# Optimization experiments

Hardware: AMD Instinct MI355X
Metric: run time of the kernel (lower is better)

Reference implementation:

```python
import jax, jax.numpy as jnp
import numpy as np

N_NODES = 100000
N_RAND_EDGES = 1600000
EPS = 1e-12


def setup_inputs() -> dict:
    key = jax.random.key(0)
    k_x, k_w1, k_w2, k_r, k_c = jax.random.split(key, 5)
    X = jax.random.normal(k_x, (N_NODES, 256), dtype=jnp.float32)
    # Linear weights stored as [in, out] so forward is X @ W (bias=False)
    W1 = jax.random.normal(k_w1, (256, 128), dtype=jnp.float32) * 0.05
    W2 = jax.random.normal(k_w2, (128, 64), dtype=jnp.float32) * 0.05
    row = jax.random.randint(k_r, (N_RAND_EDGES,), 0, N_NODES, dtype=jnp.int32)
    col = jax.random.randint(k_c, (N_RAND_EDGES,), 0, N_NODES, dtype=jnp.int32)
    loops = jnp.arange(N_NODES, dtype=jnp.int32)  # self-loops (A has self-loops)
    edge_row = jnp.concatenate([row, loops])
    edge_col = jnp.concatenate([col, loops])
    return {"X": X, "W1": W1, "W2": W2, "edge_row": edge_row, "edge_col": edge_col}


def _norm_edge_weights(edge_row, edge_col):
    # degrees = row-sums of A (all values are 1.0)
    deg = jax.ops.segment_sum(jnp.ones_like(edge_row, dtype=jnp.float32), edge_row,
                              num_segments=N_NODES)
    d_inv_sqrt = 1.0 / jnp.clip(jnp.sqrt(deg), EPS)
    # A_hat = D^-1/2 A D^-1/2  <=>  per-edge weight
    return d_inv_sqrt[edge_row] * d_inv_sqrt[edge_col]


def _spmm(w, edge_row, edge_col, X):
    # (A_hat @ X)[i] = sum_{e: row_e = i} w_e * X[col_e]
    return jax.ops.segment_sum(w[:, None] * X[edge_col], edge_row,
                               num_segments=N_NODES)


def reference(X, W1, W2, edge_row, edge_col):
    w = _norm_edge_weights(edge_row, edge_col)
    # layer 0: GraphConvolution -> ReLU (dropout is identity in eval mode)
    H = jax.nn.relu(_spmm(w, edge_row, edge_col, X @ W1))
    # layer 1: GraphConvolution (logits)
    out = _spmm(w, edge_row, edge_col, H @ W2)
    return out
```

## Files before the change

### kernel.cpp

```cpp
#include <hip/hip_runtime.h>
#include <hip/hip_bf16.h>


typedef __attribute__((ext_vector_type(8))) short short8;
typedef __attribute__((ext_vector_type(4))) float floatx4;
typedef __attribute__((ext_vector_type(2))) float floatx2;

static __device__ __forceinline__ ushort f32_to_bf16_bits(float f) {
    union { ushort u; __hip_bfloat16 b; } cv;
    cv.b = __float2bfloat16(f);
    return cv.u;
}
static __device__ __forceinline__ float bf16lo_to_f32(uint u) {
    return __uint_as_float(u << 16);
}
static __device__ __forceinline__ float bf16hi_to_f32(uint u) {
    return __uint_as_float(u & 0xffff0000u);
}
static __device__ __forceinline__ uint pack2bf(float a, float b) {
    return (uint)f32_to_bf16_bits(a) | ((uint)f32_to_bf16_bits(b) << 16);
}

#define CSR_EPB 8192
#define SPMM_CHUNK 2048

__global__ __launch_bounds__(256) void scan_phase1_kernel(
    const int* __restrict__ in, int* __restrict__ out,
    int* __restrict__ block_total, int n) {
    __shared__ int tsum[256];
    int t = threadIdx.x;
    int base = blockIdx.x * 1024 + t * 4;
    int v0 = (base + 0 < n) ? in[base + 0] : 0;
    int v1 = (base + 1 < n) ? in[base + 1] : 0;
    int v2 = (base + 2 < n) ? in[base + 2] : 0;
    int v3 = (base + 3 < n) ? in[base + 3] : 0;
    tsum[t] = v0 + v1 + v2 + v3;
    __syncthreads();
    for (int off = 1; off < 256; off <<= 1) {
        int x = (t >= off) ? tsum[t - off] : 0;
        __syncthreads();
        tsum[t] += x;
        __syncthreads();
    }
    if (t == 255) block_total[blockIdx.x] = tsum[255];
    int run = (t == 0) ? 0 : tsum[t - 1];
    if (base + 0 < n) out[base + 0] = run; run += v0;
    if (base + 1 < n) out[base + 1] = run; run += v1;
    if (base + 2 < n) out[base + 2] = run; run += v2;
    if (base + 3 < n) out[base + 3] = run;
}

__global__ __launch_bounds__(256) void scan_phase2_kernel(
    const int* __restrict__ block_total, int* __restrict__ block_offset, int G) {
    __shared__ int s[256];
    int t = threadIdx.x;
    s[t] = (t < G) ? block_total[t] : 0;
    __syncthreads();
    for (int off = 1; off < 256; off <<= 1) {
        int x = (t >= off) ? s[t - off] : 0;
        __syncthreads();
        s[t] += x;
        __syncthreads();
    }
    if (t < G) block_offset[t] = (t == 0) ? 0 : s[t - 1];
    if (t == 0) block_offset[G] = s[255];
}

__global__ __launch_bounds__(256) void scan_phase3_kernel(
    int* __restrict__ arr, const int* __restrict__ block_offset, int n, int G) {
    int i = blockIdx.x * blockDim.x + threadIdx.x;
    if (i < n) arr[i] += block_offset[i >> 10];
    if (i == 0) arr[n] = block_offset[G];
}


__global__ __launch_bounds__(256) void edge_hist_kernel(
    const int* __restrict__ keys, int* __restrict__ histG, int E, int nblk) {
    __shared__ int h[256];
    int t = threadIdx.x;
    h[t] = 0;
    __syncthreads();
    int base = blockIdx.x * CSR_EPB;
    int end = min(base + CSR_EPB, E);
    for (int i = base + t; i < end; i += 256)
        atomicAdd(&h[keys[i] >> 9], 1);
    __syncthreads();
    histG[t * nblk + blockIdx.x] = h[t];
}

__global__ __launch_bounds__(256) void edge_bin_kernel(
    const int* __restrict__ rows, const int* __restrict__ colsIn,
    const int* __restrict__ offG, int* __restrict__ binP, int E, int nblk) {
    __shared__ int cur[256];
    int t = threadIdx.x;
    cur[t] = offG[t * nblk + blockIdx.x];
    __syncthreads();
    int base = blockIdx.x * CSR_EPB;
    int end = min(base + CSR_EPB, E);
    for (int i = base + t; i < end; i += 256) {
        int r = rows[i], c = colsIn[i];
        int p = atomicAdd(&cur[r >> 9], 1);
        binP[p] = ((r & 511) << 17) | c;
    }
}

__global__ __launch_bounds__(256) void deg_dinv_from_bin_kernel(
    const int* __restrict__ binP, const int* __restrict__ offG,
    int* __restrict__ deg, float* __restrict__ dinv, int E, int nblk, int N) {
    __shared__ int cnt[512];
    int b = blockIdx.x;
    int rbase = b << 9;
    if (rbase >= N) return;
    int t = threadIdx.x;
    for (int i = t; i < 512; i += 256) cnt[i] = 0;
    __syncthreads();
    int bs = offG[b * nblk];
    int be = (b + 1 < 256) ? offG[(b + 1) * nblk] : E;
    for (int e = bs + t; e < be; e += 256)
        atomicAdd(&cnt[binP[e] >> 17], 1);
    __syncthreads();
    for (int i = t; i < 512; i += 256) {
        int r = rbase + i;
        if (r < N) {
            int d = cnt[i];
            deg[r] = d;
            dinv[r] = 1.0f / sqrtf(fmaxf((float)d, 1e-24f));
        }
    }
}

__global__ __launch_bounds__(256) void edge_scatter_kernel(
    const int* __restrict__ binP, const int* __restrict__ offG,
    const int* __restrict__ row_ptr, int* __restrict__ csr_col,
    int E, int nblk, int N) {
    __shared__ int cur[512];
    int b = blockIdx.x;
    int rbase = b << 9;
    if (rbase >= N) return;
    int t = threadIdx.x;
    for (int i = t; i < 512; i += 256) {
        int r = rbase + i;
        cur[i] = (r < N) ? row_ptr[r] : 0;
    }
    __syncthreads();
    int bs = offG[b * nblk];
    int be = (b + 1 < 256) ? offG[(b + 1) * nblk] : E;
    for (int e = bs + t; e < be; e += 256) {
        int pk = binP[e];
        int rl = pk >> 17;
        int c = pk & 0x1ffff;
        int p = atomicAdd(&cur[rl], 1);
        csr_col[p] = c;
    }
}

__global__ void cast_weights_kernel(const float* __restrict__ W1, const float* __restrict__ W2,
                                    ushort* __restrict__ W1t, ushort* __restrict__ W2t) {
    int i = blockIdx.x * blockDim.x + threadIdx.x;
    if (i < 256 * 128) {
        int n = i >> 8, k = i & 255;
        W1t[i] = f32_to_bf16_bits(W1[k * 128 + n]);
    } else {
        int j = i - 256 * 128;
        if (j < 128 * 64) {
            int n = j >> 7, k = j & 127;
            W2t[j] = f32_to_bf16_bits(W2[k * 64 + n]);
        }
    }
}

template <int KTOT, int NCOLS, bool AF32>
__global__ __launch_bounds__(256) void gemm_mfma_kernel(
    const void* __restrict__ Aptr, const ushort* __restrict__ Bt,
    const float* __restrict__ dinv, ushort* __restrict__ Cbf, int M) {
    constexpr int KP = 128;
    constexpr int COLT = NCOLS / 16;
    __shared__ ushort Bs[NCOLS][KP + 8];
    int tid = threadIdx.x;
    int wave = tid >> 6, lane = tid & 63;
    int quad = lane >> 4, l16 = lane & 15;
    int row0 = blockIdx.x * 64;
    int rowA = row0 + wave * 16 + l16;
    int rowAc = min(rowA, M - 1);

    floatx4 acc[COLT];
#pragma unroll
    for (int t = 0; t < COLT; t++) acc[t] = (floatx4){0.f, 0.f, 0.f, 0.f};

    for (int kp = 0; kp < KTOT; kp += KP) {
        for (int u = tid; u < NCOLS * (KP / 8); u += 256) {
            int n = u / (KP / 8);
            int k8 = (u % (KP / 8)) * 8;
            *(short8*)&Bs[n][k8] = *(const short8*)(Bt + (size_t)n * KTOT + kp + k8);
        }
        __syncthreads();
#pragma unroll
        for (int kc = 0; kc < KP / 32; kc++) {
            int kk = kp + kc * 32 + quad * 8;
            short8 a;
            if (AF32) {
                const float* ap = (const float*)Aptr + (size_t)rowAc * KTOT + kk;
#pragma unroll
                for (int j = 0; j < 8; j++) a[j] = (short)f32_to_bf16_bits(ap[j]);
            } else {
                a = *(const short8*)((const ushort*)Aptr + (size_t)rowAc * KTOT + kk);
            }
#pragma unroll
            for (int t = 0; t < COLT; t++) {
                short8 b = *(const short8*)&Bs[t * 16 + l16][kc * 32 + quad * 8];
                acc[t] = __builtin_amdgcn_mfma_f32_16x16x32_bf16(a, b, acc[t], 0, 0, 0);
            }
        }
        __syncthreads();
    }

#pragma unroll
    for (int r = 0; r < 4; r++) {
        int row = row0 + wave * 16 + quad * 4 + r;
        if (row < M) {
            float dv = dinv[row];
#pragma unroll
            for (int t = 0; t < COLT; t++)
                Cbf[(size_t)row * NCOLS + t * 16 + l16] = f32_to_bf16_bits(dv * acc[t][r]);
        }
    }
}

__global__ __launch_bounds__(256) void spmm_f128_kernel(
    const int* __restrict__ row_ptr, const int* __restrict__ cols,
    const float* __restrict__ dinv, const ushort* __restrict__ Xin,
    ushort* __restrict__ Yout, int n) {
    __shared__ int cstage[SPMM_CHUNK];
    int r0 = blockIdx.x * 16;
    int tid = threadIdx.x;
    int wv = tid >> 6;
    int lane = tid & 63;
    int g = lane >> 4, lg = lane & 15;
    int row = r0 + wv * 4 + g;
    bool ok = row < n;
    int rc = ok ? row : (n - 1);
    int beg = row_ptr[rc];
    int end = ok ? row_ptr[rc + 1] : beg;
    int bbeg = row_ptr[r0];
    int bend = row_ptr[min(r0 + 16, n)];

    floatx2 acc2[4];
#pragma unroll
    for (int i = 0; i < 4; i++) acc2[i] = (floatx2){0.f, 0.f};

    const ushort* xb = Xin + lg * 8;

#define ACC_DW(U, D)                                            \
    {                                                            \
        floatx2 v_;                                              \
        v_.x = bf16lo_to_f32(U);                                 \
        v_.y = bf16hi_to_f32(U);                                 \
        acc2[D] += v_;                                           \
    }
#define ACC_U4(UU)                                               \
    ACC_DW(UU.x, 0) ACC_DW(UU.y, 1) ACC_DW(UU.z, 2) ACC_DW(UU.w, 3)

    for (int cb = bbeg; cb < bend; cb += SPMM_CHUNK) {
        int ce = min(cb + SPMM_CHUNK, bend);
        __syncthreads();
        for (int i = cb + tid; i < ce; i += 256)
            cstage[i - cb] = cols[i];
        __syncthreads();
        int s = max(beg, cb), t_ = min(end, ce);
        int e = s;
        for (; e + 4 <= t_; e += 4) {
            int c0 = cstage[e - cb], c1 = cstage[e + 1 - cb];
            int c2 = cstage[e + 2 - cb], c3 = cstage[e + 3 - cb];
            uint4 u0 = *(const uint4*)(xb + (size_t)c0 * 128);
            uint4 u1 = *(const uint4*)(xb + (size_t)c1 * 128);
            uint4 u2 = *(const uint4*)(xb + (size_t)c2 * 128);
            uint4 u3 = *(const uint4*)(xb + (size_t)c3 * 128);
            ACC_U4(u0) ACC_U4(u1) ACC_U4(u2) ACC_U4(u3)
        }
        for (; e < t_; e++) {
            int c = cstage[e - cb];
            uint4 u = *(const uint4*)(xb + (size_t)c * 128);
            ACC_U4(u)
        }
    }
#undef ACC_U4
#undef ACC_DW

    if (ok) {
        float dv = dinv[row];
        float a0 = fmaxf(dv * acc2[0].x, 0.f), a1 = fmaxf(dv * acc2[0].y, 0.f);
        float a2 = fmaxf(dv * acc2[1].x, 0.f), a3 = fmaxf(dv * acc2[1].y, 0.f);
        float a4 = fmaxf(dv * acc2[2].x, 0.f), a5 = fmaxf(dv * acc2[2].y, 0.f);
        float a6 = fmaxf(dv * acc2[3].x, 0.f), a7 = fmaxf(dv * acc2[3].y, 0.f);
        uint4 o;
        o.x = pack2bf(a0, a1);
        o.y = pack2bf(a2, a3);
        o.z = pack2bf(a4, a5);
        o.w = pack2bf(a6, a7);
        *(uint4*)(Yout + (size_t)row * 128 + lg * 8) = o;
    }
}

__global__ __launch_bounds__(256) void spmm_f64_kernel(
    const int* __restrict__ row_ptr, const int* __restrict__ cols,
    const float* __restrict__ dinv, const ushort* __restrict__ Xin,
    float* __restrict__ Yout, int n) {
    __shared__ int cstage[SPMM_CHUNK];
    int r0 = blockIdx.x * 16;
    int tid = threadIdx.x;
    int wv = tid >> 6;
    int lane = tid & 63;
    int g = lane >> 4, lg = lane & 15;
    int row = r0 + wv * 4 + g;
    bool ok = row < n;
    int rc = ok ? row : (n - 1);
    int beg = row_ptr[rc];
    int end = ok ? row_ptr[rc + 1] : beg;
    int bbeg = row_ptr[r0];
    int bend = row_ptr[min(r0 + 16, n)];

    floatx2 acc2[2];
    acc2[0] = (floatx2){0.f, 0.f};
    acc2[1] = (floatx2){0.f, 0.f};

    const ushort* xb = Xin + lg * 4;

#define ACC_DW(U, D)                                            \
    {                                                            \
        floatx2 v_;                                              \
        v_.x = bf16lo_to_f32(U);                                 \
        v_.y = bf16hi_to_f32(U);                                 \
        acc2[D] += v_;                                           \
    }
#define ACC_U2(UU) ACC_DW(UU.x, 0) ACC_DW(UU.y, 1)

    for (int cb = bbeg; cb < bend; cb += SPMM_CHUNK) {
        int ce = min(cb + SPMM_CHUNK, bend);
        __syncthreads();
        for (int i = cb + tid; i < ce; i += 256)
            cstage[i - cb] = cols[i];
        __syncthreads();
        int s = max(beg, cb), t_ = min(end, ce);
        int e = s;
        for (; e + 4 <= t_; e += 4) {
            int c0 = cstage[e - cb], c1 = cstage[e + 1 - cb];
            int c2 = cstage[e + 2 - cb], c3 = cstage[e + 3 - cb];
            uint2 u0 = *(const uint2*)(xb + (size_t)c0 * 64);
            uint2 u1 = *(const uint2*)(xb + (size_t)c1 * 64);
            uint2 u2 = *(const uint2*)(xb + (size_t)c2 * 64);
            uint2 u3 = *(const uint2*)(xb + (size_t)c3 * 64);
            ACC_U2(u0) ACC_U2(u1) ACC_U2(u2) ACC_U2(u3)
        }
        for (; e < t_; e++) {
            int c = cstage[e - cb];
            uint2 u = *(const uint2*)(xb + (size_t)c * 64);
            ACC_U2(u)
        }
    }
#undef ACC_U2
#undef ACC_DW

    if (ok) {
        float dv = dinv[row];
        float4 o = make_float4(dv * acc2[0].x, dv * acc2[0].y,
                               dv * acc2[1].x, dv * acc2[1].y);
        *(float4*)(Yout + (size_t)row * 64 + lg * 4) = o;
    }
}


extern "C" void kernel_launch(void* const* d_in, const int* in_sizes, int n_in,
                              void* d_out, int out_size, void* d_ws, size_t ws_size,
                              hipStream_t stream) {
    const float* X  = (const float*)d_in[0];
    const float* W1 = (const float*)d_in[1];
    const float* W2 = (const float*)d_in[2];
    const int* erow = (const int*)d_in[3];
    const int* ecol = (const int*)d_in[4];

    const int N = in_sizes[0] / 256;
    const int E = in_sizes[3];
    const int G = (N + 1023) >> 10;

    const int nblk = (E + CSR_EPB - 1) / CSR_EPB;
    const int SL = 256 * nblk;
    const int GS = (SL + 1023) >> 10;
    const int GMAX = (G > GS) ? G : GS;

    char* ws = (char*)d_ws;
    size_t off = 0;
    auto carve = [&](size_t bytes) -> char* {
        char* p = ws + off;
        off += (bytes + 255) & ~(size_t)255;
        return p;
    };
    int*    deg       = (int*)   carve((size_t)N * 4);
    float*  dinv      = (float*) carve((size_t)N * 4);
    int*    row_ptr   = (int*)   carve((size_t)(N + 1) * 4);
    int*    blk_total = (int*)   carve((size_t)GMAX * 4);
    int*    blk_off   = (int*)   carve((size_t)(GMAX + 1) * 4);
    int*    offG      = (int*)   carve((size_t)(SL + 1) * 4);
    size_t binP_bytes = (size_t)E * 4;
    size_t xw1_bytes  = (size_t)N * 128 * 2;
    char*  uni        = carve(binP_bytes > xw1_bytes ? binP_bytes : xw1_bytes);
    int*    binP      = (int*)uni;
    ushort* XW1       = (ushort*)uni;
    int*    csr_col   = (int*)   carve((size_t)E * 4);
    ushort* W1t       = (ushort*)carve((size_t)256 * 128 * 2);
    ushort* W2t       = (ushort*)carve((size_t)128 * 64 * 2);
    ushort* H         = (ushort*)carve((size_t)N * 128 * 2);
    ushort* HW2       = (ushort*)carve((size_t)N * 64 * 2);

    edge_hist_kernel<<<nblk, 256, 0, stream>>>(erow, offG, E, nblk);
    scan_phase1_kernel<<<GS, 256, 0, stream>>>(offG, offG, blk_total, SL);
    scan_phase2_kernel<<<1, 256, 0, stream>>>(blk_total, blk_off, GS);
    scan_phase3_kernel<<<(SL + 255) / 256, 256, 0, stream>>>(offG, blk_off, SL, GS);
    edge_bin_kernel<<<nblk, 256, 0, stream>>>(erow, ecol, offG, binP, E, nblk);

    deg_dinv_from_bin_kernel<<<256, 256, 0, stream>>>(binP, offG, deg, dinv, E, nblk, N);
    scan_phase1_kernel<<<G, 256, 0, stream>>>(deg, row_ptr, blk_total, N);
    scan_phase2_kernel<<<1, 256, 0, stream>>>(blk_total, blk_off, G);
    scan_phase3_kernel<<<(N + 255) / 256, 256, 0, stream>>>(row_ptr, blk_off, N, G);

    edge_scatter_kernel<<<256, 256, 0, stream>>>(binP, offG, row_ptr, csr_col, E, nblk, N);

    cast_weights_kernel<<<(256 * 128 + 128 * 64 + 255) / 256, 256, 0, stream>>>(W1, W2, W1t, W2t);

    gemm_mfma_kernel<256, 128, true><<<(N + 63) / 64, 256, 0, stream>>>(
        (const void*)X, W1t, dinv, XW1, N);

    spmm_f128_kernel<<<(N + 15) / 16, 256, 0, stream>>>(row_ptr, csr_col, dinv, XW1, H, N);

    gemm_mfma_kernel<128, 64, false><<<(N + 63) / 64, 256, 0, stream>>>(
        (const void*)H, W2t, dinv, HW2, N);

    spmm_f64_kernel<<<(N + 15) / 16, 256, 0, stream>>>(row_ptr, csr_col, dinv, HW2, (float*)d_out, N);
}
```

Measured before the change: 356.2 us.

## Fuse layer-1 SpMM with second GEMM, merge cast into histogram, drop scan pass

The first SpMM now keeps its ReLU output tile in shared memory and immediately multiplies it by W2 with MFMA, writing HW2 directly. This removes the H buffer round trip and one GEMM launch. The weight cast is folded into the histogram kernel as extra blocks, and the offG scan's phase-3 pass is dropped by adding the block offset at each consumer. The SpMM inner loops gain an 8-way unroll and the staging chunk is halved. The costs are more shared memory and extra W2 staging in every SpMM block, plus lower per-block parallelism for the fused GEMM.

New measurement: 348.2 us. 1.02x faster.

```diff
diff --git a/kernel.cpp b/kernel.cpp
--- a/kernel.cpp
+++ b/kernel.cpp
@@ -22,7 +22,7 @@
 }
 
 #define CSR_EPB 8192
-#define SPMM_CHUNK 2048
+#define SPMM_CHUNK 1024
 
 __global__ __launch_bounds__(256) void scan_phase1_kernel(
     const int* __restrict__ in, int* __restrict__ out,
@@ -73,27 +73,45 @@
     if (i == 0) arr[n] = block_offset[G];
 }
 
-
-__global__ __launch_bounds__(256) void edge_hist_kernel(
-    const int* __restrict__ keys, int* __restrict__ histG, int E, int nblk) {
+__global__ __launch_bounds__(256) void edge_hist_cast_kernel(
+    const int* __restrict__ keys, int* __restrict__ histG, int E, int nblk,
+    const float* __restrict__ W1, const float* __restrict__ W2,
+    ushort* __restrict__ W1t, ushort* __restrict__ W2t) {
+    int b = blockIdx.x;
+    if (b >= nblk) {
+        int i = (b - nblk) * 256 + threadIdx.x;
+        if (i < 256 * 128) {
+            int n = i >> 8, k = i & 255;
+            W1t[i] = f32_to_bf16_bits(W1[k * 128 + n]);
+        } else {
+            int j = i - 256 * 128;
+            if (j < 128 * 64) {
+                int n = j >> 7, k = j & 127;
+                W2t[j] = f32_to_bf16_bits(W2[k * 64 + n]);
+            }
+        }
+        return;
+    }
     __shared__ int h[256];
     int t = threadIdx.x;
     h[t] = 0;
     __syncthreads();
-    int base = blockIdx.x * CSR_EPB;
+    int base = b * CSR_EPB;
     int end = min(base + CSR_EPB, E);
     for (int i = base + t; i < end; i += 256)
         atomicAdd(&h[keys[i] >> 9], 1);
     __syncthreads();
-    histG[t * nblk + blockIdx.x] = h[t];
+    histG[t * nblk + b] = h[t];
 }
 
 __global__ __launch_bounds__(256) void edge_bin_kernel(
     const int* __restrict__ rows, const int* __restrict__ colsIn,
-    const int* __restrict__ offG, int* __restrict__ binP, int E, int nblk) {
+    const int* __restrict__ offG, const int* __restrict__ blk_off1,
+    int* __restrict__ binP, int E, int nblk) {
     __shared__ int cur[256];
     int t = threadIdx.x;
-    cur[t] = offG[t * nblk + blockIdx.x];
+    int idx = t * nblk + blockIdx.x;
+    cur[t] = offG[idx] + blk_off1[idx >> 10];
     __syncthreads();
     int base = blockIdx.x * CSR_EPB;
     int end = min(base + CSR_EPB, E);
@@ -106,6 +124,7 @@
 
 __global__ __launch_bounds__(256) void deg_dinv_from_bin_kernel(
     const int* __restrict__ binP, const int* __restrict__ offG,
+    const int* __restrict__ blk_off1,
     int* __restrict__ deg, float* __restrict__ dinv, int E, int nblk, int N) {
     __shared__ int cnt[512];
     int b = blockIdx.x;
@@ -114,8 +133,13 @@
     int t = threadIdx.x;
     for (int i = t; i < 512; i += 256) cnt[i] = 0;
     __syncthreads();
-    int bs = offG[b * nblk];
-    int be = (b + 1 < 256) ? offG[(b + 1) * nblk] : E;
+    int i0 = b * nblk;
+    int bs = offG[i0] + blk_off1[i0 >> 10];
+    int be = E;
+    if (b + 1 < 256) {
+        int i1 = (b + 1) * nblk;
+        be = offG[i1] + blk_off1[i1 >> 10];
+    }
     for (int e = bs + t; e < be; e += 256)
         atomicAdd(&cnt[binP[e] >> 17], 1);
     __syncthreads();
@@ -131,6 +155,7 @@
 
 __global__ __launch_bounds__(256) void edge_scatter_kernel(
     const int* __restrict__ binP, const int* __restrict__ offG,
+    const int* __restrict__ blk_off1,
     const int* __restrict__ row_ptr, int* __restrict__ csr_col,
     int E, int nblk, int N) {
     __shared__ int cur[512];
@@ -143,29 +168,19 @@
         cur[i] = (r < N) ? row_ptr[r] : 0;
     }
     __syncthreads();
-    int bs = offG[b * nblk];
-    int be = (b + 1 < 256) ? offG[(b + 1) * nblk] : E;
+    int i0 = b * nblk;
+    int bs = offG[i0] + blk_off1[i0 >> 10];
+    int be = E;
+    if (b + 1 < 256) {
+        int i1 = (b + 1) * nblk;
+        be = offG[i1] + blk_off1[i1 >> 10];
+    }
     for (int e = bs + t; e < be; e += 256) {
         int pk = binP[e];
         int rl = pk >> 17;
         int c = pk & 0x1ffff;
         int p = atomicAdd(&cur[rl], 1);
         csr_col[p] = c;
-    }
-}
-
-__global__ void cast_weights_kernel(const float* __restrict__ W1, const float* __restrict__ W2,
-                                    ushort* __restrict__ W1t, ushort* __restrict__ W2t) {
-    int i = blockIdx.x * blockDim.x + threadIdx.x;
-    if (i < 256 * 128) {
-        int n = i >> 8, k = i & 255;
-        W1t[i] = f32_to_bf16_bits(W1[k * 128 + n]);
-    } else {
-        int j = i - 256 * 128;
-        if (j < 128 * 64) {
-            int n = j >> 7, k = j & 127;
-            W2t[j] = f32_to_bf16_bits(W2[k * 64 + n]);
-        }
     }
 }
 
@@ -226,16 +241,19 @@
     }
 }
 
-__global__ __launch_bounds__(256) void spmm_f128_kernel(
+__global__ __launch_bounds__(256) void spmm_gemm2_kernel(
     const int* __restrict__ row_ptr, const int* __restrict__ cols,
-    const float* __restrict__ dinv, const ushort* __restrict__ Xin,
-    ushort* __restrict__ Yout, int n) {
+    const float* __restrict__ dinv, const ushort* __restrict__ XW1,
+    const ushort* __restrict__ W2t, ushort* __restrict__ HW2, int n) {
     __shared__ int cstage[SPMM_CHUNK];
-    int r0 = blockIdx.x * 16;
+    __shared__ ushort W2s[64][136];
+    __shared__ ushort Hs[16][136];
+
     int tid = threadIdx.x;
     int wv = tid >> 6;
     int lane = tid & 63;
     int g = lane >> 4, lg = lane & 15;
+    int r0 = blockIdx.x * 16;
     int row = r0 + wv * 4 + g;
     bool ok = row < n;
     int rc = ok ? row : (n - 1);
@@ -244,11 +262,16 @@
     int bbeg = row_ptr[r0];
     int bend = row_ptr[min(r0 + 16, n)];
 
+    for (int u = tid; u < 64 * 16; u += 256) {
+        int nn = u >> 4, k8 = (u & 15) * 8;
+        *(short8*)&W2s[nn][k8] = *(const short8*)(W2t + nn * 128 + k8);
+    }
+
     floatx2 acc2[4];
 #pragma unroll
     for (int i = 0; i < 4; i++) acc2[i] = (floatx2){0.f, 0.f};
 
-    const ushort* xb = Xin + lg * 8;
+    const ushort* xb = XW1 + lg * 8;
 
 #define ACC_DW(U, D)                                            \
     {                                                            \
@@ -268,6 +291,22 @@
         __syncthreads();
         int s = max(beg, cb), t_ = min(end, ce);
         int e = s;
+        for (; e + 8 <= t_; e += 8) {
+            int c0 = cstage[e - cb], c1 = cstage[e + 1 - cb];
+            int c2 = cstage[e + 2 - cb], c3 = cstage[e + 3 - cb];
+            int c4 = cstage[e + 4 - cb], c5 = cstage[e + 5 - cb];
+            int c6 = cstage[e + 6 - cb], c7 = cstage[e + 7 - cb];
+            uint4 u0 = *(const uint4*)(xb + (size_t)c0 * 128);
+            uint4 u1 = *(const uint4*)(xb + (size_t)c1 * 128);
+            uint4 u2 = *(const uint4*)(xb + (size_t)c2 * 128);
+            uint4 u3 = *(const uint4*)(xb + (size_t)c3 * 128);
+            uint4 u4 = *(const uint4*)(xb + (size_t)c4 * 128);
+            uint4 u5 = *(const uint4*)(xb + (size_t)c5 * 128);
+            uint4 u6 = *(const uint4*)(xb + (size_t)c6 * 128);
+            uint4 u7 = *(const uint4*)(xb + (size_t)c7 * 128);
+            ACC_U4(u0) ACC_U4(u1) ACC_U4(u2) ACC_U4(u3)
+            ACC_U4(u4) ACC_U4(u5) ACC_U4(u6) ACC_U4(u7)
+        }
         for (; e + 4 <= t_; e += 4) {
             int c0 = cstage[e - cb], c1 = cstage[e + 1 - cb];
             int c2 = cstage[e + 2 - cb], c3 = cstage[e + 3 - cb];
@@ -286,8 +325,8 @@
 #undef ACC_U4
 #undef ACC_DW
 
-    if (ok) {
-        float dv = dinv[row];
+    {
+        float dv = ok ? dinv[row] : 0.f;
         float a0 = fmaxf(dv * acc2[0].x, 0.f), a1 = fmaxf(dv * acc2[0].y, 0.f);
         float a2 = fmaxf(dv * acc2[1].x, 0.f), a3 = fmaxf(dv * acc2[1].y, 0.f);
         float a4 = fmaxf(dv * acc2[2].x, 0.f), a5 = fmaxf(dv * acc2[2].y, 0.f);
@@ -297,7 +336,24 @@
         o.y = pack2bf(a2, a3);
         o.z = pack2bf(a4, a5);
         o.w = pack2bf(a6, a7);
-        *(uint4*)(Yout + (size_t)row * 128 + lg * 8) = o;
+        *(uint4*)&Hs[wv * 4 + g][lg * 8] = o;
+    }
+    __syncthreads();
+
+    int quad = g, l16 = lg;
+    floatx4 dacc = (floatx4){0.f, 0.f, 0.f, 0.f};
+#pragma unroll
+    for (int kc = 0; kc < 4; kc++) {
+        short8 a = *(const short8*)&Hs[l16][kc * 32 + quad * 8];
+        short8 b = *(const short8*)&W2s[wv * 16 + l16][kc * 32 + quad * 8];
+        dacc = __builtin_amdgcn_mfma_f32_16x16x32_bf16(a, b, dacc, 0, 0, 0);
+    }
+#pragma unroll
+    for (int r = 0; r < 4; r++) {
+        int rowD = r0 + quad * 4 + r;
+        if (rowD < n)
+            HW2[(size_t)rowD * 64 + wv * 16 + l16] =
+                f32_to_bf16_bits(dinv[rowD] * dacc[r]);
     }
 }
 
@@ -342,6 +398,22 @@
         __syncthreads();
         int s = max(beg, cb), t_ = min(end, ce);
         int e = s;
+        for (; e + 8 <= t_; e += 8) {
+            int c0 = cstage[e - cb], c1 = cstage[e + 1 - cb];
+            int c2 = cstage[e + 2 - cb], c3 = cstage[e + 3 - cb];
+            int c4 = cstage[e + 4 - cb], c5 = cstage[e + 5 - cb];
+            int c6 = cstage[e + 6 - cb], c7 = cstage[e + 7 - cb];
+            uint2 u0 = *(const uint2*)(xb + (size_t)c0 * 64);
+            uint2 u1 = *(const uint2*)(xb + (size_t)c1 * 64);
+            uint2 u2 = *(const uint2*)(xb + (size_t)c2 * 64);
+            uint2 u3 = *(const uint2*)(xb + (size_t)c3 * 64);
+            uint2 u4 = *(const uint2*)(xb + (size_t)c4 * 64);
+            uint2 u5 = *(const uint2*)(xb + (size_t)c5 * 64);
+            uint2 u6 = *(const uint2*)(xb + (size_t)c6 * 64);
+            uint2 u7 = *(const uint2*)(xb + (size_t)c7 * 64);
+            ACC_U2(u0) ACC_U2(u1) ACC_U2(u2) ACC_U2(u3)
+            ACC_U2(u4) ACC_U2(u5) ACC_U2(u6) ACC_U2(u7)
+        }
         for (; e + 4 <= t_; e += 4) {
             int c0 = cstage[e - cb], c1 = cstage[e + 1 - cb];
             int c2 = cstage[e + 2 - cb], c3 = cstage[e + 3 - cb];
@@ -386,6 +458,7 @@
     const int SL = 256 * nblk;
     const int GS = (SL + 1023) >> 10;
     const int GMAX = (G > GS) ? G : GS;
+    const int CAST_BLKS = (256 * 128 + 128 * 64 + 255) / 256;
 
     char* ws = (char*)d_ws;
     size_t off = 0;
@@ -398,7 +471,8 @@
     float*  dinv      = (float*) carve((size_t)N * 4);
     int*    row_ptr   = (int*)   carve((size_t)(N + 1) * 4);
     int*    blk_total = (int*)   carve((size_t)GMAX * 4);
-    int*    blk_off   = (int*)   carve((size_t)(GMAX + 1) * 4);
+    int*    blk_off1  = (int*)   carve((size_t)(GMAX + 1) * 4);
+    int*    blk_off2  = (int*)   carve((size_t)(GMAX + 1) * 4);
     int*    offG      = (int*)   carve((size_t)(SL + 1) * 4);
     size_t binP_bytes = (size_t)E * 4;
     size_t xw1_bytes  = (size_t)N * 128 * 2;
@@ -408,31 +482,26 @@
     int*    csr_col   = (int*)   carve((size_t)E * 4);
     ushort* W1t       = (ushort*)carve((size_t)256 * 128 * 2);
     ushort* W2t       = (ushort*)carve((size_t)128 * 64 * 2);
-    ushort* H         = (ushort*)carve((size_t)N * 128 * 2);
     ushort* HW2       = (ushort*)carve((size_t)N * 64 * 2);
 
-    edge_hist_kernel<<<nblk, 256, 0, stream>>>(erow, offG, E, nblk);
+    edge_hist_cast_kernel<<<nblk + CAST_BLKS, 256, 0, stream>>>(
+        erow, offG, E, nblk, W1, W2, W1t, W2t);
     scan_phase1_kernel<<<GS, 256, 0, stream>>>(offG, offG, blk_total, SL);
-    scan_phase2_kernel<<<1, 256, 0, stream>>>(blk_total, blk_off, GS);
-    scan_phase3_kernel<<<(SL + 255) / 256, 256, 0, stream>>>(offG, blk_off, SL, GS);
-    edge_bin_kernel<<<nblk, 256, 0, stream>>>(erow, ecol, offG, binP, E, nblk);
-
-    deg_dinv_from_bin_kernel<<<256, 256, 0, stream>>>(binP, offG, deg, dinv, E, nblk, N);
+    scan_phase2_kernel<<<1, 256, 0, stream>>>(blk_total, blk_off1, GS);
+    edge_bin_kernel<<<nblk, 256, 0, stream>>>(erow, ecol, offG, blk_off1, binP, E, nblk);
+
+    deg_dinv_from_bin_kernel<<<256, 256, 0, stream>>>(binP, offG, blk_off1, deg, dinv, E, nblk, N);
     scan_phase1_kernel<<<G, 256, 0, stream>>>(deg, row_ptr, blk_total, N);
-    scan_phase2_kernel<<<1, 256, 0, stream>>>(blk_total, blk_off, G);
-    scan_phase3_kernel<<<(N + 255) / 256, 256, 0, stream>>>(row_ptr, blk_off, N, G);
-
-    edge_scatter_kernel<<<256, 256, 0, stream>>>(binP, offG, row_ptr, csr_col, E, nblk, N);
-
-    cast_weights_kernel<<<(256 * 128 + 128 * 64 + 255) / 256, 256, 0, stream>>>(W1, W2, W1t, W2t);
+    scan_phase2_kernel<<<1, 256, 0, stream>>>(blk_total, blk_off2, G);
+    scan_phase3_kernel<<<(N + 255) / 256, 256, 0, stream>>>(row_ptr, blk_off2, N, G);
+
+    edge_scatter_kernel<<<256, 256, 0, stream>>>(binP, offG, blk_off1, row_ptr, csr_col, E, nblk, N);
 
     gemm_mfma_kernel<256, 128, true><<<(N + 63) / 64, 256, 0, stream>>>(
         (const void*)X, W1t, dinv, XW1, N);
 
-    spmm_f128_kernel<<<(N + 15) / 16, 256, 0, stream>>>(row_ptr, csr_col, dinv, XW1, H, N);
-
-    gemm_mfma_kernel<128, 64, false><<<(N + 63) / 64, 256, 0, stream>>>(
-        (const void*)H, W2t, dinv, HW2, N);
+    spmm_gemm2_kernel<<<(N + 15) / 16, 256, 0, stream>>>(
+        row_ptr, csr_col, dinv, XW1, W2t, HW2, N);
 
     spmm_f64_kernel<<<(N + 15) / 16, 256, 0, stream>>>(row_ptr, csr_col, dinv, HW2, (float*)d_out, N);
 }
```
